# Kernel tuning notes

Hardware: AMD Instinct MI355X
Metric: run time of the kernel (lower is better)

The kernel has to match this reference:

```python
import jax, jax.numpy as jnp
import numpy as np

WINDOW_SIZE = 256
NEG_INF = jnp.finfo(jnp.float32).min


def setup_inputs() -> dict:
    key = jax.random.key(0)
    kq, kk, kv = jax.random.split(key, 3)
    B, H, S, D = 1, 8, 4096, 128
    q = jax.random.normal(kq, (B, H, S, D), dtype=jnp.float32)
    k = jax.random.normal(kk, (B, H, S, D), dtype=jnp.float32)
    v = jax.random.normal(kv, (B, H, S, D), dtype=jnp.float32)
    return {"q": q, "k": k, "v": v}


def _local_mask(seq_len: int) -> jnp.ndarray:
    idx = jnp.arange(seq_len)
    qi = idx[:, None]
    ki = idx[None, :]
    # causal AND within trailing window of WINDOW_SIZE keys
    return (ki <= qi) & (ki >= qi - WINDOW_SIZE + 1)  # [S, S] bool


def reference(q, k, v):
    B, H, S, D = q.shape
    scale = 1.0 / np.sqrt(D).astype(np.float32)
    mask = _local_mask(S)  # [S, S]
    scores = jnp.einsum('bhsd,bhtd->bhst', q, k) * scale  # [B,H,S,S]
    scores = jnp.where(mask[None, None, :, :], scores, NEG_INF)
    attn = jax.nn.softmax(scores.astype(jnp.float32), axis=-1).astype(q.dtype)
    out = jnp.einsum('bhst,bhtd->bhsd', attn, v)
    return out
```

## Files before the change

### kernel.cpp

```cpp
#include <hip/hip_runtime.h>


typedef short  bf16x8 __attribute__((ext_vector_type(8)));
typedef __bf16 bf16v8 __attribute__((ext_vector_type(8)));
typedef float  f32x4  __attribute__((ext_vector_type(4)));

constexpr int QB = 64, DH = 128, WIN = 256, KT = 64;
constexpr int NTILE = 5, NSUB = 20;
constexpr float SCALE = 0.08838834764831844f;

constexpr int KLO_OFF = 16384;
constexpr int PSTR    = 328;
constexpr int VT_OFF  = 43008;
constexpr int SMEM_BYTES = VT_OFF + 16384;

__device__ __forceinline__ short bf16_of(float x) {
  union { float f; unsigned u; } a; a.f = x;
  unsigned r = a.u + 0x7fffu + ((a.u >> 16) & 1u);
  return (short)(r >> 16);
}
__device__ __forceinline__ float f_of(short s) {
  union { float f; unsigned u; } a; a.u = ((unsigned)(unsigned short)s) << 16;
  return a.f;
}
__device__ __forceinline__ bf16v8 as_bf(bf16x8 s) {
  union { bf16x8 s; bf16v8 b; } u; u.s = s; return u.b;
}
#define MFMA(A, B, C) __builtin_amdgcn_mfma_f32_16x16x32_bf16(as_bf(A), as_bf(B), (C), 0, 0, 0)

__global__ __launch_bounds__(256, 2)
void lwa_mfma(const float* __restrict__ qg, const float* __restrict__ kg,
              const float* __restrict__ vg, float* __restrict__ og, int S) {
  __shared__ __align__(16) char smem[SMEM_BYTES];

  const int h   = blockIdx.y;
  const int q0  = blockIdx.x * QB;
  const int tid = threadIdx.x;
  const int wv  = tid >> 6;
  const int lane = tid & 63;
  const int lg  = lane >> 4;
  const int lm  = lane & 15;

  const float* qb = qg + ((size_t)h * S) * DH;
  const float* kb = kg + ((size_t)h * S) * DH;
  const float* vb = vg + ((size_t)h * S) * DH;

  bf16x8 qhi[4], qlo[4];
  {
    const float* qrow = qb + ((size_t)(q0 + 16 * wv + lm)) * DH;
#pragma unroll
    for (int kc = 0; kc < 4; ++kc) {
      const int d0 = 32 * kc + 8 * lg;
      float4 a = *(const float4*)(qrow + d0);
      float4 b = *(const float4*)(qrow + d0 + 4);
      float x[8] = {a.x, a.y, a.z, a.w, b.x, b.y, b.z, b.w};
      bf16x8 hi, lo;
#pragma unroll
      for (int j = 0; j < 8; ++j) {
        float xs = x[j] * SCALE;
        short hs = bf16_of(xs);
        hi[j] = hs;
        lo[j] = bf16_of(xs - f_of(hs));
      }
      qhi[kc] = hi; qlo[kc] = lo;
    }
  }

  f32x4 acc[NSUB];
#pragma unroll
  for (int t = 0; t < NSUB; ++t) acc[t] = (f32x4){0.f, 0.f, 0.f, 0.f};

  const int srow = tid >> 4;
  const int sd0  = 8 * (tid & 15);

  for (int t = 0; t < NTILE; ++t) {
    const int kt0 = q0 - WIN + t * KT;
    if (kt0 < 0) continue;
    __syncthreads();
#pragma unroll
    for (int i = 0; i < 4; ++i) {
      const int row = srow + 16 * i;
      const float* kr = kb + ((size_t)(kt0 + row)) * DH + sd0;
      float4 a = *(const float4*)(kr);
      float4 b = *(const float4*)(kr + 4);
      float x[8] = {a.x, a.y, a.z, a.w, b.x, b.y, b.z, b.w};
      bf16x8 hi, lo;
#pragma unroll
      for (int j = 0; j < 8; ++j) {
        short hs = bf16_of(x[j]);
        hi[j] = hs;
        lo[j] = bf16_of(x[j] - f_of(hs));
      }
      const int byte = row * 256 + ((sd0 * 2) ^ ((row & 15) << 4));
      *(bf16x8*)(smem + byte) = hi;
      *(bf16x8*)(smem + KLO_OFF + byte) = lo;
    }
    __syncthreads();
#pragma unroll
    for (int n = 0; n < 4; ++n) {
      f32x4 c = acc[4 * t + n];
#pragma unroll
      for (int kc = 0; kc < 4; ++kc) {
        const int key = 16 * n + lm;
        const int byte = key * 256 + (((64 * kc) + 16 * lg) ^ (lm << 4));
        bf16x8 kh = *(const bf16x8*)(smem + byte);
        bf16x8 kl = *(const bf16x8*)(smem + KLO_OFF + byte);
        c = MFMA(qhi[kc], kh, c);
        c = MFMA(qlo[kc], kh, c);
        c = MFMA(qhi[kc], kl, c);
      }
      acc[4 * t + n] = c;
    }
  }
  __syncthreads();

  float rl[4];
#pragma unroll
  for (int r = 0; r < 4; ++r) {
    const int qi = q0 + 16 * wv + 4 * lg + r;
    float m = -3.0e38f;
#pragma unroll
    for (int ts = 0; ts < NSUB; ++ts) {
      const int ki = q0 - WIN + 16 * ts + lm;
      const bool ok = (ki >= 0) && (ki <= qi) && (ki > qi - WIN);
      float s = ok ? acc[ts][r] : -3.0e38f;
      acc[ts][r] = s;
      m = fmaxf(m, s);
    }
#pragma unroll
    for (int msk = 1; msk < 16; msk <<= 1) m = fmaxf(m, __shfl_xor(m, msk));
    float l = 0.f;
#pragma unroll
    for (int ts = 0; ts < NSUB; ++ts) {
      float p = __expf(acc[ts][r] - m);
      acc[ts][r] = p;
      l += p;
    }
#pragma unroll
    for (int msk = 1; msk < 16; msk <<= 1) l += __shfl_xor(l, msk);
    rl[r] = 1.f / l;
  }

#pragma unroll
  for (int ts = 0; ts < NSUB; ++ts)
#pragma unroll
    for (int r = 0; r < 4; ++r) {
      const int row = 16 * wv + 4 * lg + r;
      const int col = 16 * ts + lm;
      *(short*)(smem + row * (PSTR * 2) + col * 2) = bf16_of(acc[ts][r]);
    }

  f32x4 o[8];
#pragma unroll
  for (int n = 0; n < 8; ++n) o[n] = (f32x4){0.f, 0.f, 0.f, 0.f};

  for (int t = 0; t < NTILE; ++t) {
    const int kt0 = q0 - WIN + t * KT;
    if (kt0 < 0) continue;
    __syncthreads();
#pragma unroll
    for (int i = 0; i < 4; ++i) {
      const int key = srow + 16 * i;
      const float* vr = vb + ((size_t)(kt0 + key)) * DH + sd0;
      float4 a = *(const float4*)(vr);
      float4 b = *(const float4*)(vr + 4);
      float x[8] = {a.x, a.y, a.z, a.w, b.x, b.y, b.z, b.w};
#pragma unroll
      for (int j = 0; j < 8; ++j) {
        const int d = sd0 + j;
        const int swz = ((d & 7) ^ ((d >> 3) & 7)) << 4;
        const int byte = d * 128 + ((key * 2) ^ swz);
        *(short*)(smem + VT_OFF + byte) = bf16_of(x[j]);
      }
    }
    __syncthreads();
#pragma unroll
    for (int kc = 0; kc < 2; ++kc) {
      const int colb = (16 * wv + lm) * (PSTR * 2) + 128 * t + 64 * kc + 16 * lg;
      bf16x8 pf = *(const bf16x8*)(smem + colb);
#pragma unroll
      for (int n = 0; n < 8; ++n) {
        const int d = 16 * n + lm;
        const int swz = ((d & 7) ^ ((d >> 3) & 7)) << 4;
        const int byte = d * 128 + ((64 * kc + 16 * lg) ^ swz);
        bf16x8 vf = *(const bf16x8*)(smem + VT_OFF + byte);
        o[n] = MFMA(pf, vf, o[n]);
      }
    }
  }

  float* orow = og + ((size_t)(h * S + q0 + 16 * wv)) * DH;
#pragma unroll
  for (int n = 0; n < 8; ++n)
#pragma unroll
    for (int r = 0; r < 4; ++r)
      orow[(4 * lg + r) * DH + 16 * n + lm] = o[n][r] * rl[r];
}

extern "C" void kernel_launch(void* const* d_in, const int* in_sizes, int n_in,
                              void* d_out, int out_size, void* d_ws, size_t ws_size,
                              hipStream_t stream) {
  const float* q = (const float*)d_in[0];
  const float* k = (const float*)d_in[1];
  const float* v = (const float*)d_in[2];
  float* out = (float*)d_out;
  const int H = 8, D = 128;
  const int S = in_sizes[0] / (H * D);
  dim3 grid(S / QB, H);
  lwa_mfma<<<grid, 256, 0, stream>>>(q, k, v, out, S);
}
```

Baseline: 112.1 us.

## Load K directly into registers and double-buffer prefetched V tiles

The QK^T phase now reads K rows straight from global memory into registers and splits them into bf16 hi/lo there, removing the K shared-memory staging and its barriers. Each wave reloads K rows independently, which adds redundant global/L2 traffic. The V tiles are prefetched into registers two tiles ahead, overlapping with the softmax, and written into a double-buffered LDS region, which adds register pressure and shared memory. The grid is flattened with heads interleaved so neighbouring blocks share L2 locality differently.

```diff
diff --git a/kernel.cpp b/kernel.cpp
--- a/kernel.cpp
+++ b/kernel.cpp
@@ -9,10 +9,10 @@
 constexpr int NTILE = 5, NSUB = 20;
 constexpr float SCALE = 0.08838834764831844f;
 
-constexpr int KLO_OFF = 16384;
-constexpr int PSTR    = 328;
-constexpr int VT_OFF  = 43008;
-constexpr int SMEM_BYTES = VT_OFF + 16384;
+constexpr int PSTR = 328;
+constexpr int VT0  = 43008;
+constexpr int VT1  = VT0 + 16384;
+constexpr int SMEM_BYTES = VT1 + 16384;
 
 __device__ __forceinline__ short bf16_of(float x) {
   union { float f; unsigned u; } a; a.f = x;
@@ -29,25 +29,26 @@
 #define MFMA(A, B, C) __builtin_amdgcn_mfma_f32_16x16x32_bf16(as_bf(A), as_bf(B), (C), 0, 0, 0)
 
 __global__ __launch_bounds__(256, 2)
-void lwa_mfma(const float* __restrict__ qg, const float* __restrict__ kg,
-              const float* __restrict__ vg, float* __restrict__ og, int S) {
+void lwa3(const float* __restrict__ qg, const float* __restrict__ kg,
+          const float* __restrict__ vg, float* __restrict__ og, int S) {
   __shared__ __align__(16) char smem[SMEM_BYTES];
 
-  const int h   = blockIdx.y;
-  const int q0  = blockIdx.x * QB;
+  const int bid = blockIdx.x;
+  const int h   = bid & 7;
+  const int q0  = (bid >> 3) * QB;
   const int tid = threadIdx.x;
   const int wv  = tid >> 6;
   const int lane = tid & 63;
   const int lg  = lane >> 4;
   const int lm  = lane & 15;
 
-  const float* qb = qg + ((size_t)h * S) * DH;
-  const float* kb = kg + ((size_t)h * S) * DH;
-  const float* vb = vg + ((size_t)h * S) * DH;
+  const float* qgb = qg + (size_t)h * S * DH;
+  const float* kgb = kg + (size_t)h * S * DH;
+  const float* vgb = vg + (size_t)h * S * DH;
 
   bf16x8 qhi[4], qlo[4];
   {
-    const float* qrow = qb + ((size_t)(q0 + 16 * wv + lm)) * DH;
+    const float* qrow = qgb + (size_t)(q0 + 16 * wv + lm) * DH;
 #pragma unroll
     for (int kc = 0; kc < 4; ++kc) {
       const int d0 = 32 * kc + 8 * lg;
@@ -70,41 +71,32 @@
 #pragma unroll
   for (int t = 0; t < NSUB; ++t) acc[t] = (f32x4){0.f, 0.f, 0.f, 0.f};
 
-  const int srow = tid >> 4;
-  const int sd0  = 8 * (tid & 15);
-
+#pragma unroll
   for (int t = 0; t < NTILE; ++t) {
     const int kt0 = q0 - WIN + t * KT;
     if (kt0 < 0) continue;
-    __syncthreads();
-#pragma unroll
-    for (int i = 0; i < 4; ++i) {
-      const int row = srow + 16 * i;
-      const float* kr = kb + ((size_t)(kt0 + row)) * DH + sd0;
-      float4 a = *(const float4*)(kr);
-      float4 b = *(const float4*)(kr + 4);
-      float x[8] = {a.x, a.y, a.z, a.w, b.x, b.y, b.z, b.w};
-      bf16x8 hi, lo;
-#pragma unroll
-      for (int j = 0; j < 8; ++j) {
-        short hs = bf16_of(x[j]);
-        hi[j] = hs;
-        lo[j] = bf16_of(x[j] - f_of(hs));
-      }
-      const int byte = row * 256 + ((sd0 * 2) ^ ((row & 15) << 4));
-      *(bf16x8*)(smem + byte) = hi;
-      *(bf16x8*)(smem + KLO_OFF + byte) = lo;
-    }
-    __syncthreads();
 #pragma unroll
     for (int n = 0; n < 4; ++n) {
+      const float* krow = kgb + (size_t)(kt0 + 16 * n + lm) * DH;
+      float4 kfa[4], kfb[4];
+#pragma unroll
+      for (int kc = 0; kc < 4; ++kc) {
+        const int d0 = 32 * kc + 8 * lg;
+        kfa[kc] = *(const float4*)(krow + d0);
+        kfb[kc] = *(const float4*)(krow + d0 + 4);
+      }
       f32x4 c = acc[4 * t + n];
 #pragma unroll
       for (int kc = 0; kc < 4; ++kc) {
-        const int key = 16 * n + lm;
-        const int byte = key * 256 + (((64 * kc) + 16 * lg) ^ (lm << 4));
-        bf16x8 kh = *(const bf16x8*)(smem + byte);
-        bf16x8 kl = *(const bf16x8*)(smem + KLO_OFF + byte);
+        float x[8] = {kfa[kc].x, kfa[kc].y, kfa[kc].z, kfa[kc].w,
+                      kfb[kc].x, kfb[kc].y, kfb[kc].z, kfb[kc].w};
+        bf16x8 kh, kl;
+#pragma unroll
+        for (int j = 0; j < 8; ++j) {
+          short hs = bf16_of(x[j]);
+          kh[j] = hs;
+          kl[j] = bf16_of(x[j] - f_of(hs));
+        }
         c = MFMA(qhi[kc], kh, c);
         c = MFMA(qlo[kc], kh, c);
         c = MFMA(qhi[kc], kl, c);
@@ -112,7 +104,36 @@
       acc[4 * t + n] = c;
     }
   }
-  __syncthreads();
+
+  const int srow = tid >> 4;
+  const int sd0  = (tid & 15) * 8;
+  auto vload = [&](int kt0, float4 r[8]) {
+#pragma unroll
+    for (int i = 0; i < 4; ++i) {
+      const float* p = vgb + (size_t)(kt0 + srow + 16 * i) * DH + sd0;
+      r[2 * i]     = *(const float4*)(p);
+      r[2 * i + 1] = *(const float4*)(p + 4);
+    }
+  };
+  auto vwrite = [&](char* dst, const float4 r[8]) {
+#pragma unroll
+    for (int i = 0; i < 4; ++i) {
+      const int key = srow + 16 * i;
+      float x[8] = {r[2*i].x, r[2*i].y, r[2*i].z, r[2*i].w,
+                    r[2*i+1].x, r[2*i+1].y, r[2*i+1].z, r[2*i+1].w};
+#pragma unroll
+      for (int j = 0; j < 8; ++j) {
+        const int d = sd0 + j;
+        const int swz = ((d & 7) ^ ((d >> 3) & 7)) << 4;
+        *(short*)(dst + d * 128 + ((key * 2) ^ swz)) = bf16_of(x[j]);
+      }
+    }
+  };
+
+  const int kt0_0 = q0 - WIN, kt0_1 = q0 - WIN + KT;
+  float4 vr0[8], vr1[8];
+  if (kt0_0 >= 0) vload(kt0_0, vr0);
+  if (kt0_1 >= 0) vload(kt0_1, vr1);
 
   float rl[4];
 #pragma unroll
@@ -150,42 +171,40 @@
       *(short*)(smem + row * (PSTR * 2) + col * 2) = bf16_of(acc[ts][r]);
     }
 
+  if (kt0_0 >= 0) vwrite(smem + VT0, vr0);
+  if (kt0_1 >= 0) vwrite(smem + VT1, vr1);
+  __syncthreads();
+
   f32x4 o[8];
 #pragma unroll
   for (int n = 0; n < 8; ++n) o[n] = (f32x4){0.f, 0.f, 0.f, 0.f};
 
+#pragma unroll
   for (int t = 0; t < NTILE; ++t) {
     const int kt0 = q0 - WIN + t * KT;
-    if (kt0 < 0) continue;
-    __syncthreads();
-#pragma unroll
-    for (int i = 0; i < 4; ++i) {
-      const int key = srow + 16 * i;
-      const float* vr = vb + ((size_t)(kt0 + key)) * DH + sd0;
-      float4 a = *(const float4*)(vr);
-      float4 b = *(const float4*)(vr + 4);
-      float x[8] = {a.x, a.y, a.z, a.w, b.x, b.y, b.z, b.w};
-#pragma unroll
-      for (int j = 0; j < 8; ++j) {
-        const int d = sd0 + j;
-        const int swz = ((d & 7) ^ ((d >> 3) & 7)) << 4;
-        const int byte = d * 128 + ((key * 2) ^ swz);
-        *(short*)(smem + VT_OFF + byte) = bf16_of(x[j]);
-      }
-    }
-    __syncthreads();
-#pragma unroll
-    for (int kc = 0; kc < 2; ++kc) {
-      const int colb = (16 * wv + lm) * (PSTR * 2) + 128 * t + 64 * kc + 16 * lg;
-      bf16x8 pf = *(const bf16x8*)(smem + colb);
-#pragma unroll
-      for (int n = 0; n < 8; ++n) {
-        const int d = 16 * n + lm;
-        const int swz = ((d & 7) ^ ((d >> 3) & 7)) << 4;
-        const int byte = d * 128 + ((64 * kc + 16 * lg) ^ swz);
-        bf16x8 vf = *(const bf16x8*)(smem + VT_OFF + byte);
-        o[n] = MFMA(pf, vf, o[n]);
-      }
+    const int tp  = t + 2;
+    const int ktp = q0 - WIN + tp * KT;
+    float4 pre[8];
+    if (tp < NTILE && ktp >= 0) vload(ktp, pre);
+    if (kt0 >= 0) {
+      const char* vbuf = smem + ((t & 1) ? VT1 : VT0);
+#pragma unroll
+      for (int kc = 0; kc < 2; ++kc) {
+        const int colb = (16 * wv + lm) * (PSTR * 2) + 128 * t + 64 * kc + 16 * lg;
+        bf16x8 pf = *(const bf16x8*)(smem + colb);
+#pragma unroll
+        for (int n = 0; n < 8; ++n) {
+          const int d = 16 * n + lm;
+          const int swz = ((d & 7) ^ ((d >> 3) & 7)) << 4;
+          bf16x8 vf = *(const bf16x8*)(vbuf + d * 128 + ((64 * kc + 16 * lg) ^ swz));
+          o[n] = MFMA(pf, vf, o[n]);
+        }
+      }
+    }
+    if (tp < NTILE) {
+      __syncthreads();
+      if (ktp >= 0) vwrite(smem + ((t & 1) ? VT1 : VT0), pre);
+      __syncthreads();
     }
   }
 
@@ -206,6 +225,6 @@
   float* out = (float*)d_out;
   const int H = 8, D = 128;
   const int S = in_sizes[0] / (H * D);
-  dim3 grid(S / QB, H);
-  lwa_mfma<<<grid, 256, 0, stream>>>(q, k, v, out, S);
-}
+  const int nblk = (S / QB) * H;
+  lwa3<<<dim3(nblk), 256, 0, stream>>>(q, k, v, out, S);
+}
```

Measured after the change: 130.9 us. +16.7%, slower.
